# Kernel optimization log

Measured on AMD Instinct MI355X. Metric: run time of the kernel, lower is better.

## Reference

```python
import jax, jax.numpy as jnp
import numpy as np

B, T, D = 16, 2000, 512
L_ORDER, R_ORDER = 10, 5
L_STRIDE, R_STRIDE = 2, 2
KERNEL_RES = True


def setup_inputs() -> dict:
    key = jax.random.key(0)
    k1, k2 = jax.random.split(key)
    inputs = jax.random.normal(k1, (B, T, D), dtype=jnp.float32)
    filt = jax.random.normal(k2, (L_ORDER + R_ORDER + 1, D), dtype=jnp.float32)
    return {"inputs": inputs, "filt": filt}


def reference(inputs, filt):
    # FSMN memory block: strided dilated depthwise conv over time.
    # inputs: (B, T, D); filt: (l_order + r_order + 1, D)
    batch, frames, dims = inputs.shape
    L = L_ORDER * L_STRIDE  # left zero-pad
    R = R_ORDER * R_STRIDE  # right zero-pad
    x = jnp.pad(inputs, ((0, 0), (L, R), (0, 0)))

    # center tap
    out = inputs * filt[L_ORDER]
    # left taps: tap k sits at (frame - (l_order - k) * l_stride) in the
    # unpadded signal -> offset k*l_stride in the padded signal.
    for k in range(L_ORDER):
        off = k * L_STRIDE
        out = out + x[:, off:off + frames] * filt[k]
    # right taps: tap k sits at frame + 1 + k*r_stride -> padded offset L+1+k*r_stride.
    for k in range(R_ORDER):
        off = L + 1 + k * R_STRIDE
        out = out + x[:, off:off + frames] * filt[L_ORDER + 1 + k]

    if KERNEL_RES:
        out = out + inputs
    return out
```

## Files before the change

kernel.cpp:

```cpp
#include <hip/hip_runtime.h>
#include <hip/hip_bf16.h>


constexpr int B = 16;
constexpr int T = 2000;
constexpr int D = 512;
constexpr int NTAP = 16;
constexpr int S = 50;
constexpr int NSTRIP = T / S;
constexpr int ITERS = S / 2;
constexpr int NXCD = 8;

__global__ __launch_bounds__(256) void fsmn_sw_kernel(
    const float* __restrict__ x,
    const float* __restrict__ filt,
    float* __restrict__ out)
{
    const int nbl = B * 2 * NSTRIP;
    const int cpx = nbl / NXCD;
    int bid = blockIdx.x;
    bid = (bid & (NXCD - 1)) * cpx + (bid >> 3);

    const int strip = bid % NSTRIP;
    const int bd    = bid / NSTRIP;
    const int dhalf = bd & 1;
    const int b     = bd >> 1;
    const int d     = dhalf * 256 + (int)threadIdx.x;
    const int t0    = strip * S;

    const float* xp = x + (size_t)(b * T) * D + d;
    float*       op = out + (size_t)(b * T + t0) * D + d;

    float F[NTAP];
#pragma unroll
    for (int k = 0; k < NTAP; ++k) F[k] = filt[k * D + d];
    F[10] += 1.0f;

    float W[32];
#pragma unroll
    for (int m = 0; m < 32; ++m) {
        const int p = t0 - 20 + m;
        W[m] = (p >= 0) ? xp[p * D] : 0.0f;
    }

#pragma unroll
    for (int i = 0; i < ITERS; ++i) {
        const int j = (2 * i) & 31;
        float a0 = W[j] * F[0];
        float a1 = W[(j + 1) & 31] * F[0];

        if (i + 1 < ITERS) {
            const int p0 = t0 + 2 * i + 12;
            const int p1 = p0 + 1;
            W[j]            = (p0 < T) ? xp[p0 * D] : 0.0f;
            W[(j + 1) & 31] = (p1 < T) ? xp[p1 * D] : 0.0f;
        }

#pragma unroll
        for (int k = 1; k <= 10; ++k) {
            a0 = fmaf(W[(j + 2 * k) & 31],     F[k], a0);
            a1 = fmaf(W[(j + 1 + 2 * k) & 31], F[k], a1);
        }
#pragma unroll
        for (int k = 11; k <= 15; ++k) {
            a0 = fmaf(W[(j + 2 * k - 1) & 31], F[k], a0);
            a1 = fmaf(W[(j + 2 * k) & 31],     F[k], a1);
        }

        op[(2 * i) * D]     = a0;
        op[(2 * i + 1) * D] = a1;
    }
}

extern "C" void kernel_launch(void* const* d_in, const int* in_sizes, int n_in,
                              void* d_out, int out_size, void* d_ws, size_t ws_size,
                              hipStream_t stream) {
    const float* x    = (const float*)d_in[0];
    const float* filt = (const float*)d_in[1];
    float* out        = (float*)d_out;

    const int grid = B * 2 * NSTRIP;
    fsmn_sw_kernel<<<grid, 256, 0, stream>>>(x, filt, out);
}
```

Measured before the change: 29.99 us.

## Deepen register ring prefetch distance and use nontemporal output stores

Enlarges the register ring buffer so input rows are loaded several iterations ahead instead of one, giving global loads more time to land before the FMAs consume them. Output writes switch to nontemporal stores to avoid polluting cache with streamed results. The cost is more live registers per thread, which may reduce occupancy.

```diff
diff --git a/kernel.cpp b/kernel.cpp
--- a/kernel.cpp
+++ b/kernel.cpp
@@ -10,6 +10,8 @@
 constexpr int NSTRIP = T / S;
 constexpr int ITERS = S / 2;
 constexpr int NXCD = 8;
+constexpr int P = 4;
+constexpr int RING = 32 + 2 * (P - 1);
 
 __global__ __launch_bounds__(256) void fsmn_sw_kernel(
     const float* __restrict__ x,
@@ -36,39 +38,39 @@
     for (int k = 0; k < NTAP; ++k) F[k] = filt[k * D + d];
     F[10] += 1.0f;
 
-    float W[32];
+    float W[RING];
 #pragma unroll
-    for (int m = 0; m < 32; ++m) {
+    for (int m = 0; m < RING; ++m) {
         const int p = t0 - 20 + m;
-        W[m] = (p >= 0) ? xp[p * D] : 0.0f;
+        W[m] = (p >= 0 && p < T) ? xp[p * D] : 0.0f;
     }
 
 #pragma unroll
     for (int i = 0; i < ITERS; ++i) {
-        const int j = (2 * i) & 31;
-        float a0 = W[j] * F[0];
-        float a1 = W[(j + 1) & 31] * F[0];
+        const int base = (2 * i) % RING;
+        float a0 = W[base] * F[0];
+        float a1 = W[(base + 1) % RING] * F[0];
 
-        if (i + 1 < ITERS) {
-            const int p0 = t0 + 2 * i + 12;
+        if (i + P < ITERS) {
+            const int p0 = t0 + 18 + 2 * i;
             const int p1 = p0 + 1;
-            W[j]            = (p0 < T) ? xp[p0 * D] : 0.0f;
-            W[(j + 1) & 31] = (p1 < T) ? xp[p1 * D] : 0.0f;
+            W[base]              = (p0 < T) ? xp[p0 * D] : 0.0f;
+            W[(base + 1) % RING] = (p1 < T) ? xp[p1 * D] : 0.0f;
         }
 
 #pragma unroll
         for (int k = 1; k <= 10; ++k) {
-            a0 = fmaf(W[(j + 2 * k) & 31],     F[k], a0);
-            a1 = fmaf(W[(j + 1 + 2 * k) & 31], F[k], a1);
+            a0 = fmaf(W[(base + 2 * k) % RING],     F[k], a0);
+            a1 = fmaf(W[(base + 1 + 2 * k) % RING], F[k], a1);
         }
 #pragma unroll
         for (int k = 11; k <= 15; ++k) {
-            a0 = fmaf(W[(j + 2 * k - 1) & 31], F[k], a0);
-            a1 = fmaf(W[(j + 2 * k) & 31],     F[k], a1);
+            a0 = fmaf(W[(base + 2 * k - 1) % RING], F[k], a0);
+            a1 = fmaf(W[(base + 2 * k) % RING],     F[k], a1);
         }
 
-        op[(2 * i) * D]     = a0;
-        op[(2 * i + 1) * D] = a1;
+        __builtin_nontemporal_store(a0, &op[(2 * i) * D]);
+        __builtin_nontemporal_store(a1, &op[(2 * i + 1) * D]);
     }
 }
 
```

Result: faster. 28.84 us (-3.8%).

## Vectorize to float2 per thread, shrink time strips, use nontemporal stores

Applied to the files above, without the earlier changes.

Each thread now handles two adjacent channels via float2 loads, so one block covers all 512 channels. Strips shrink from 50 to 10 frames, which means the full 39-frame window is loaded up front with no rolling refill. Outputs are written with nontemporal stores. The goal is wider memory transactions and more parallel blocks. The cost is roughly 4x halo re-reads of the input per output frame and higher register use per thread.

```diff
diff --git a/kernel.cpp b/kernel.cpp
--- a/kernel.cpp
+++ b/kernel.cpp
@@ -2,83 +2,88 @@
 #include <hip/hip_bf16.h>
 
 
+typedef float f32x2 __attribute__((ext_vector_type(2)));
+
 constexpr int B = 16;
 constexpr int T = 2000;
 constexpr int D = 512;
+constexpr int D2 = D / 2;
 constexpr int NTAP = 16;
-constexpr int S = 50;
+constexpr int S = 10;
 constexpr int NSTRIP = T / S;
 constexpr int ITERS = S / 2;
+constexpr int WSPAN = 39;
 constexpr int NXCD = 8;
 
-__global__ __launch_bounds__(256) void fsmn_sw_kernel(
-    const float* __restrict__ x,
-    const float* __restrict__ filt,
-    float* __restrict__ out)
+__global__ __launch_bounds__(256, 4) void fsmn_f2_kernel(
+    const f32x2* __restrict__ x,
+    const f32x2* __restrict__ filt,
+    f32x2* __restrict__ out)
 {
-    const int nbl = B * 2 * NSTRIP;
+    const int nbl = B * NSTRIP;
     const int cpx = nbl / NXCD;
     int bid = blockIdx.x;
     bid = (bid & (NXCD - 1)) * cpx + (bid >> 3);
 
     const int strip = bid % NSTRIP;
-    const int bd    = bid / NSTRIP;
-    const int dhalf = bd & 1;
-    const int b     = bd >> 1;
-    const int d     = dhalf * 256 + (int)threadIdx.x;
+    const int b     = bid / NSTRIP;
+    const int d2    = (int)threadIdx.x;
     const int t0    = strip * S;
+    const int rowbase = b * T;
 
-    const float* xp = x + (size_t)(b * T) * D + d;
-    float*       op = out + (size_t)(b * T + t0) * D + d;
+    f32x2 F[NTAP];
+#pragma unroll
+    for (int k = 0; k < NTAP; ++k) F[k] = filt[k * D2 + d2];
+    F[10].x += 1.0f;
+    F[10].y += 1.0f;
 
-    float F[NTAP];
+    f32x2 W[WSPAN];
 #pragma unroll
-    for (int k = 0; k < NTAP; ++k) F[k] = filt[k * D + d];
-    F[10] += 1.0f;
+    for (int m = 0; m < WSPAN; ++m) {
+        const int p = t0 - 20 + m;
+        if (p >= 0 && p < T) {
+            W[m] = x[(rowbase + p) * D2 + d2];
+        } else {
+            W[m] = (f32x2)(0.0f);
+        }
+    }
 
-    float W[32];
-#pragma unroll
-    for (int m = 0; m < 32; ++m) {
-        const int p = t0 - 20 + m;
-        W[m] = (p >= 0) ? xp[p * D] : 0.0f;
-    }
+    f32x2* op = out + (size_t)(rowbase + t0) * D2 + d2;
 
 #pragma unroll
     for (int i = 0; i < ITERS; ++i) {
-        const int j = (2 * i) & 31;
-        float a0 = W[j] * F[0];
-        float a1 = W[(j + 1) & 31] * F[0];
-
-        if (i + 1 < ITERS) {
-            const int p0 = t0 + 2 * i + 12;
-            const int p1 = p0 + 1;
-            W[j]            = (p0 < T) ? xp[p0 * D] : 0.0f;
-            W[(j + 1) & 31] = (p1 < T) ? xp[p1 * D] : 0.0f;
-        }
+        const int s0 = 2 * i;
+        f32x2 a0, a1;
+        a0.x = W[s0].x * F[0].x;         a0.y = W[s0].y * F[0].y;
+        a1.x = W[s0 + 1].x * F[0].x;     a1.y = W[s0 + 1].y * F[0].y;
 
 #pragma unroll
         for (int k = 1; k <= 10; ++k) {
-            a0 = fmaf(W[(j + 2 * k) & 31],     F[k], a0);
-            a1 = fmaf(W[(j + 1 + 2 * k) & 31], F[k], a1);
+            a0.x = fmaf(W[s0 + 2 * k].x,     F[k].x, a0.x);
+            a0.y = fmaf(W[s0 + 2 * k].y,     F[k].y, a0.y);
+            a1.x = fmaf(W[s0 + 2 * k + 1].x, F[k].x, a1.x);
+            a1.y = fmaf(W[s0 + 2 * k + 1].y, F[k].y, a1.y);
         }
 #pragma unroll
-        for (int k = 11; k <= 15; ++k) {
-            a0 = fmaf(W[(j + 2 * k - 1) & 31], F[k], a0);
-            a1 = fmaf(W[(j + 2 * k) & 31],     F[k], a1);
+        for (int k = 0; k <= 4; ++k) {
+            a0.x = fmaf(W[s0 + 21 + 2 * k].x, F[11 + k].x, a0.x);
+            a0.y = fmaf(W[s0 + 21 + 2 * k].y, F[11 + k].y, a0.y);
+            a1.x = fmaf(W[s0 + 22 + 2 * k].x, F[11 + k].x, a1.x);
+            a1.y = fmaf(W[s0 + 22 + 2 * k].y, F[11 + k].y, a1.y);
         }
 
-        op[(2 * i) * D]     = a0;
-        op[(2 * i + 1) * D] = a1;
+        __builtin_nontemporal_store(a0, &op[(2 * i) * D2]);
+        __builtin_nontemporal_store(a1, &op[(2 * i + 1) * D2]);
     }
 }
 
 extern "C" void kernel_launch(void* const* d_in, const int* in_sizes, int n_in,
                               void* d_out, int out_size, void* d_ws, size_t ws_size,
                               hipStream_t stream) {
-    const float* x    = (const float*)d_in[0];
-    const float* filt = (const float*)d_in[1];
-    float* out        = (float*)d_out;
+    const f32x2* x    = (const f32x2*)d_in[0];
+    const f32x2* filt = (const f32x2*)d_in[1];
+    f32x2* out        = (f32x2*)d_out;
 
-    const int grid = B * 2 * NSTRIP;
-    fsmn_sw_kernel<<<grid, 256, 0, stream>>>(x, filt, out);
+    const int grid = B * NSTRIP;
+    fsmn_f2_kernel<<<grid, 256, 0, stream>>>(x, filt, out);
 }
```

Result: slower. 32.52 us (+8.4%).

## Stage input window in LDS via direct global-to-LDS loads with shorter strips

Applied to the files above, without the earlier changes.

Each block now loads its 39-row time window for 256 channels straight into shared memory with 16-byte global_load_lds transfers, then each thread copies its column into registers and computes 10 outputs. The strip length drops from 50 to 10, which gives five times as many blocks for parallelism but re-reads the 29-row halo per strip. Output stores become nontemporal. This trades a higher read amplification for vectorized, asynchronous loads and more concurrency, replacing the earlier per-thread strided scalar sliding-window loads.

```diff
diff --git a/kernel.cpp b/kernel.cpp
--- a/kernel.cpp
+++ b/kernel.cpp
@@ -2,73 +2,81 @@
 #include <hip/hip_bf16.h>
 
 
+typedef float f32x4 __attribute__((ext_vector_type(4)));
+typedef __attribute__((address_space(1))) const unsigned int gas_u32;
+typedef __attribute__((address_space(3))) unsigned int las_u32;
+
 constexpr int B = 16;
 constexpr int T = 2000;
 constexpr int D = 512;
+constexpr int DH = 256;
 constexpr int NTAP = 16;
-constexpr int S = 50;
+constexpr int S = 10;
 constexpr int NSTRIP = T / S;
-constexpr int ITERS = S / 2;
+constexpr int WROWS = 39;
 constexpr int NXCD = 8;
 
-__global__ __launch_bounds__(256) void fsmn_sw_kernel(
+__global__ __launch_bounds__(256) void fsmn_lds_kernel(
     const float* __restrict__ x,
     const float* __restrict__ filt,
     float* __restrict__ out)
 {
+    __shared__ float smem[WROWS * DH];
+
     const int nbl = B * 2 * NSTRIP;
     const int cpx = nbl / NXCD;
     int bid = blockIdx.x;
     bid = (bid & (NXCD - 1)) * cpx + (bid >> 3);
 
     const int strip = bid % NSTRIP;
-    const int bd    = bid / NSTRIP;
-    const int dhalf = bd & 1;
-    const int b     = bd >> 1;
-    const int d     = dhalf * 256 + (int)threadIdx.x;
+    const int bh    = bid / NSTRIP;
+    const int dhalf = bh & 1;
+    const int b     = bh >> 1;
     const int t0    = strip * S;
 
-    const float* xp = x + (size_t)(b * T) * D + d;
-    float*       op = out + (size_t)(b * T + t0) * D + d;
+    const int tid  = (int)threadIdx.x;
+    const int wave = tid >> 6;
+    const int lane = tid & 63;
 
+    const float* gx = x + (size_t)(b * T) * D + dhalf * DH;
+#pragma unroll
+    for (int j = 0; j < 10; ++j) {
+        const int m = wave + 4 * j;
+        if (m < WROWS) {
+            const int p = t0 - 20 + m;
+            if (p >= 0 && p < T) {
+                const float* src = gx + (size_t)p * D + lane * 4;
+                __builtin_amdgcn_global_load_lds(
+                    (gas_u32*)src,
+                    (las_u32*)&smem[m * DH],
+                    16, 0, 0);
+            } else {
+                ((f32x4*)&smem[m * DH])[lane] = (f32x4)(0.0f);
+            }
+        }
+    }
+
+    const int c = tid;
     float F[NTAP];
 #pragma unroll
-    for (int k = 0; k < NTAP; ++k) F[k] = filt[k * D + d];
+    for (int k = 0; k < NTAP; ++k) F[k] = filt[k * D + dhalf * DH + c];
     F[10] += 1.0f;
 
-    float W[32];
+    __syncthreads();
+
+    float W[WROWS];
 #pragma unroll
-    for (int m = 0; m < 32; ++m) {
-        const int p = t0 - 20 + m;
-        W[m] = (p >= 0) ? xp[p * D] : 0.0f;
-    }
+    for (int m = 0; m < WROWS; ++m) W[m] = smem[m * DH + c];
 
+    float* op = out + (size_t)(b * T + t0) * D + dhalf * DH + c;
 #pragma unroll
-    for (int i = 0; i < ITERS; ++i) {
-        const int j = (2 * i) & 31;
-        float a0 = W[j] * F[0];
-        float a1 = W[(j + 1) & 31] * F[0];
-
-        if (i + 1 < ITERS) {
-            const int p0 = t0 + 2 * i + 12;
-            const int p1 = p0 + 1;
-            W[j]            = (p0 < T) ? xp[p0 * D] : 0.0f;
-            W[(j + 1) & 31] = (p1 < T) ? xp[p1 * D] : 0.0f;
-        }
-
+    for (int i = 0; i < S; ++i) {
+        float a = W[i + 20] * F[10];
 #pragma unroll
-        for (int k = 1; k <= 10; ++k) {
-            a0 = fmaf(W[(j + 2 * k) & 31],     F[k], a0);
-            a1 = fmaf(W[(j + 1 + 2 * k) & 31], F[k], a1);
-        }
+        for (int k = 0; k < 10; ++k) a = fmaf(W[i + 2 * k], F[k], a);
 #pragma unroll
-        for (int k = 11; k <= 15; ++k) {
-            a0 = fmaf(W[(j + 2 * k - 1) & 31], F[k], a0);
-            a1 = fmaf(W[(j + 2 * k) & 31],     F[k], a1);
-        }
-
-        op[(2 * i) * D]     = a0;
-        op[(2 * i + 1) * D] = a1;
+        for (int k = 0; k < 5; ++k)  a = fmaf(W[i + 21 + 2 * k], F[11 + k], a);
+        __builtin_nontemporal_store(a, &op[(size_t)i * D]);
     }
 }
 
@@ -80,5 +88,5 @@
     float* out        = (float*)d_out;
 
     const int grid = B * 2 * NSTRIP;
-    fsmn_sw_kernel<<<grid, 256, 0, stream>>>(x, filt, out);
+    fsmn_lds_kernel<<<grid, 256, 0, stream>>>(x, filt, out);
 }
```

New measurement: 27.84 us. -7.2%, faster.
